# Kernel tuning notes

Hardware: AMD Instinct MI355X
Metric: run time of the kernel (lower is better)

The kernel has to match this reference:

```python
import jax, jax.numpy as jnp
import numpy as np

# CRPConfig defaults
KAPPA = 1.0
C = 0.95
ALPHA = 0.05
EPS = 1e-8
T_MAX = 32
MARGIN_FACTOR = 2.0

B, I, HD, L = 512, 1024, 2048, 1000


def setup_inputs() -> dict:
    key = jax.random.key(0)
    k0, k1, k2, k3 = jax.random.split(key, 4)
    x = jax.random.normal(k0, (B, I), jnp.float32)
    # kaiming-like scaling keeps activations numerically sane
    RIH = jax.random.normal(k1, (I, HD), jnp.float32) * np.float32(1.0 / np.sqrt(I))
    RH = jax.random.normal(k2, (HD, HD), jnp.float32) * np.float32(1.0 / np.sqrt(HD))
    RHL = jax.random.normal(k3, (HD, L), jnp.float32) * np.float32(1.0 / np.sqrt(HD))
    BH = jnp.zeros((HD,), jnp.float32)
    BL = jnp.zeros((L,), jnp.float32)
    MIH = jnp.ones((I, HD), jnp.float32)
    MH = jnp.ones((HD, HD), jnp.float32)
    MHL = jnp.ones((HD, L), jnp.float32)
    return {"x": x, "RIH": RIH, "RH": RH, "RHL": RHL, "BH": BH, "BL": BL,
            "MIH": MIH, "MH": MH, "MHL": MHL}


def _crp_forward(x, RIH, RH, RHL, BH, BL, MIH, MH, MHL):
    # build weights
    W_IH = RIH * MIH                      # [I, H]
    W_HL = RHL * MHL                      # [H, L]
    RHm = RH * MH                         # [H, H]
    # normalize so max column L1 <= c (value only; straight-through grad)
    col_l1 = jnp.abs(RHm).sum(axis=0)
    scale = C / jnp.maximum(col_l1.max(), EPS)
    W_H = jax.lax.stop_gradient(RHm * scale) + RHm - jax.lax.stop_gradient(RHm)

    rho = 1.0 - KAPPA + KAPPA * C
    denom = max(1e-12, 1.0 - rho)
    whl_inf = jnp.abs(W_HL).sum(axis=0).max()
    gamma_coef = whl_inf * (rho / denom)

    drive = x @ W_IH + BH                 # constant across steps, [B, H]
    Bsz = x.shape[0]
    Hs0 = jnp.zeros((Bsz, HD), x.dtype)
    active0 = jnp.ones((Bsz,), jnp.bool_)
    tau0 = jnp.full((Bsz,), T_MAX, jnp.int32)
    cert0 = jnp.zeros((Bsz,), jnp.bool_)
    logits_tau0 = jnp.zeros((Bsz, L), x.dtype)

    def step(carry, t):
        Hs, active, tau, certified, logits_tau = carry
        pre = Hs @ W_H + drive
        act = jnp.where(pre >= 0, pre, ALPHA * pre)      # LeakyReLU
        H_cand = (1.0 - KAPPA) * Hs + KAPPA * act
        H_next = jnp.where(active[:, None], H_cand, Hs)
        logits = H_next @ W_HL + BL
        # certification
        dH = jnp.max(jnp.abs(H_next - Hs), axis=1)       # H_prev == Hs
        Gamma = gamma_coef * dH
        top2 = jax.lax.top_k(logits, 2)[0]
        margin = top2[:, 0] - top2[:, 1]
        newly = active & (margin > MARGIN_FACTOR * Gamma)
        tau = jnp.where(newly, t, tau)
        certified = certified | newly
        logits_tau = jnp.where(newly[:, None], logits, logits_tau)
        active = active & (~newly)
        return (H_next, active, tau, certified, logits_tau), None

    ts = jnp.arange(1, T_MAX + 1, dtype=jnp.int32)
    (Hf, active, tau, certified, logits_tau), _ = jax.lax.scan(
        step, (Hs0, active0, tau0, cert0, logits_tau0), ts)

    never = ~certified
    logits_last = Hf @ W_HL + BL
    logits_tau = jnp.where(never[:, None], logits_last, logits_tau)
    return logits_tau


def reference(x, RIH, RH, RHL, BH, BL, MIH, MH, MHL):
    return _crp_forward(x, RIH, RH, RHL, BH, BL, MIH, MH, MHL)
```

## Files before the change

### kernel.cpp

```cpp
#include <hip/hip_runtime.h>

typedef __attribute__((ext_vector_type(8))) short short8;
typedef __attribute__((ext_vector_type(4))) float f32x4;

static constexpr int BN    = 512;
static constexpr int ID    = 1024;
static constexpr int HDm   = 2048;
static constexpr int LD    = 1000;
static constexpr int TMAXc = 32;
static constexpr float ALPHAc = 0.05f;

__device__ __forceinline__ unsigned short f2bf(float x) {
    unsigned u = __float_as_uint(x);
    u += 0x7fffu + ((u >> 16) & 1u);
    return (unsigned short)(u >> 16);
}
__device__ __forceinline__ float bf2f(unsigned short h) {
    return __uint_as_float(((unsigned)h) << 16);
}
__device__ __forceinline__ void split2(float x, unsigned short& hi, unsigned short& lo) {
    hi = f2bf(x);
    lo = f2bf(x - bf2f(hi));
}

template<bool SPLITA>
__device__ __forceinline__ void tile64x32(
    const float* __restrict__ Af,
    const unsigned short* __restrict__ Ahi, const unsigned short* __restrict__ Alo,
    int lda, int row0,
    const unsigned short* __restrict__ BThi, const unsigned short* __restrict__ BTlo,
    int ldk, int col0, int K, char* lds, f32x4& acc, int& s_out, int& p_out)
{
    char* Ah = lds;
    char* Al = lds + 16384;
    char* Bh = lds + 32768;
    char* Bl = lds + 40960;
    const int t = threadIdx.x, lane = t & 63, w = t >> 6;
    const int s = w & 7, p = w >> 3;
    s_out = s; p_out = p;
    f32x4 z = {0.f, 0.f, 0.f, 0.f};
    acc = z;

    const int ar = t >> 4, ac = (t & 15) << 3;
    const int br = t >> 5, bc = (t & 31) << 2;
    const int asb = (ar * 256 + ac * 2) ^ ((ar & 15) << 4);
    const int bsb = (br * 256 + bc * 2) ^ ((br & 15) << 4);
    const float* Ap = SPLITA ? (Af + (size_t)(row0 + ar) * lda + ac) : nullptr;
    const unsigned short* Ahp = SPLITA ? nullptr : (Ahi + (size_t)(row0 + ar) * lda + ac);
    const unsigned short* Alp = SPLITA ? nullptr : (Alo + (size_t)(row0 + ar) * lda + ac);
    const unsigned short* Bhp = BThi + (size_t)(col0 + br) * ldk + bc;
    const unsigned short* Blp = BTlo + (size_t)(col0 + br) * ldk + bc;

    const int frow = s >> 1, fcol = s & 1;
    const int arow = frow * 16 + (lane & 15);
    const int colr = fcol * 16 + (lane & 15);
    const int ab0 = arow * 256, bb0 = colr * 256;
    const int axor = (arow & 15) << 4, bxor = (colr & 15) << 4;
    const int kwin = p * 128 + ((lane >> 4) << 4);

    float4 af0a, af0b, af1a, af1b;
    uint4 ah0, al0, ah1, al1;
    if constexpr (SPLITA) {
        af0a = *(const float4*)(Ap);       af0b = *(const float4*)(Ap + 4);
        af1a = *(const float4*)(Ap + 128); af1b = *(const float4*)(Ap + 132);
    } else {
        ah0 = *(const uint4*)(Ahp);       al0 = *(const uint4*)(Alp);
        ah1 = *(const uint4*)(Ahp + 128); al1 = *(const uint4*)(Alp + 128);
    }
    uint2 bh0 = *(const uint2*)(Bhp),       bl0 = *(const uint2*)(Blp);
    uint2 bh1 = *(const uint2*)(Bhp + 128), bl1 = *(const uint2*)(Blp + 128);

    for (int k0 = 0; k0 < K; k0 += 128) {
        uint4 awh, awl;
        if constexpr (SPLITA) {
            unsigned short h[8], l[8];
            const float vv[8] = {af0a.x, af0a.y, af0a.z, af0a.w,
                                 af0b.x, af0b.y, af0b.z, af0b.w};
#pragma unroll
            for (int i = 0; i < 8; ++i) split2(vv[i], h[i], l[i]);
            awh = make_uint4((unsigned)h[0] | ((unsigned)h[1] << 16),
                             (unsigned)h[2] | ((unsigned)h[3] << 16),
                             (unsigned)h[4] | ((unsigned)h[5] << 16),
                             (unsigned)h[6] | ((unsigned)h[7] << 16));
            awl = make_uint4((unsigned)l[0] | ((unsigned)l[1] << 16),
                             (unsigned)l[2] | ((unsigned)l[3] << 16),
                             (unsigned)l[4] | ((unsigned)l[5] << 16),
                             (unsigned)l[6] | ((unsigned)l[7] << 16));
        } else { awh = ah0; awl = al0; }
        const uint2 bwh = bh0, bwl = bl0;
        __syncthreads();
        *(uint4*)(Ah + asb) = awh;
        *(uint4*)(Al + asb) = awl;
        *(uint2*)(Bh + bsb) = bwh;
        *(uint2*)(Bl + bsb) = bwl;
        if constexpr (SPLITA) { af0a = af1a; af0b = af1b; } else { ah0 = ah1; al0 = al1; }
        bh0 = bh1; bl0 = bl1;
        if (k0 + 256 < K) {
            if constexpr (SPLITA) {
                af1a = *(const float4*)(Ap + k0 + 256);
                af1b = *(const float4*)(Ap + k0 + 260);
            } else {
                ah1 = *(const uint4*)(Ahp + k0 + 256);
                al1 = *(const uint4*)(Alp + k0 + 256);
            }
            bh1 = *(const uint2*)(Bhp + k0 + 256);
            bl1 = *(const uint2*)(Blp + k0 + 256);
        }
        __syncthreads();
#pragma unroll
        for (int ks = 0; ks < 2; ++ks) {
            const int kb = kwin + ks * 64;
            short8 bh = *(const short8*)(Bh + ((bb0 + kb) ^ bxor));
            short8 bl = *(const short8*)(Bl + ((bb0 + kb) ^ bxor));
            short8 ah = *(const short8*)(Ah + ((ab0 + kb) ^ axor));
            short8 al = *(const short8*)(Al + ((ab0 + kb) ^ axor));
            acc = __builtin_amdgcn_mfma_f32_16x16x32_bf16(ah, bh, acc, 0, 0, 0);
            acc = __builtin_amdgcn_mfma_f32_16x16x32_bf16(al, bh, acc, 0, 0, 0);
            acc = __builtin_amdgcn_mfma_f32_16x16x32_bf16(ah, bl, acc, 0, 0, 0);
        }
    }
}

__device__ __forceinline__ void tile32x32(
    const unsigned short* __restrict__ Ahi, const unsigned short* __restrict__ Alo, int row0,
    const unsigned short* __restrict__ BThi, const unsigned short* __restrict__ BTlo,
    int col0, char* lds, f32x4& acc, int& s_out, int& p_out)
{
    char* Ah = lds;
    char* Al = lds + 8192;
    char* Bh = lds + 16384;
    char* Bl = lds + 24576;
    const int t = threadIdx.x, lane = t & 63, w = t >> 6;
    const int s = w & 3, p = w >> 2;
    s_out = s; p_out = p;
    f32x4 z = {0.f, 0.f, 0.f, 0.f};
    acc = z;

    const int ar = t >> 5, ac = (t & 31) << 2;
    const int asb = (ar * 256 + ac * 2) ^ ((ar & 15) << 4);
    const unsigned short* Ahp = Ahi + (size_t)(row0 + ar) * HDm + ac;
    const unsigned short* Alp = Alo + (size_t)(row0 + ar) * HDm + ac;
    const unsigned short* Bhp = BThi + (size_t)(col0 + ar) * HDm + ac;
    const unsigned short* Blp = BTlo + (size_t)(col0 + ar) * HDm + ac;

    const int frow = s >> 1, fcol = s & 1;
    const int arow = frow * 16 + (lane & 15);
    const int colr = fcol * 16 + (lane & 15);
    const int ab0 = arow * 256, bb0 = colr * 256;
    const int axor = (arow & 15) << 4, bxor = (colr & 15) << 4;
    const int kwin = p * 64 + ((lane >> 4) << 4);

    uint2 ah0 = *(const uint2*)(Ahp),       al0 = *(const uint2*)(Alp);
    uint2 bh0 = *(const uint2*)(Bhp),       bl0 = *(const uint2*)(Blp);
    uint2 ah1 = *(const uint2*)(Ahp + 128), al1 = *(const uint2*)(Alp + 128);
    uint2 bh1 = *(const uint2*)(Bhp + 128), bl1 = *(const uint2*)(Blp + 128);

    for (int k0 = 0; k0 < HDm; k0 += 128) {
        const uint2 awh = ah0, awl = al0, bwh = bh0, bwl = bl0;
        __syncthreads();
        *(uint2*)(Ah + asb) = awh;
        *(uint2*)(Al + asb) = awl;
        *(uint2*)(Bh + asb) = bwh;
        *(uint2*)(Bl + asb) = bwl;
        ah0 = ah1; al0 = al1; bh0 = bh1; bl0 = bl1;
        if (k0 + 256 < HDm) {
            ah1 = *(const uint2*)(Ahp + k0 + 256);
            al1 = *(const uint2*)(Alp + k0 + 256);
            bh1 = *(const uint2*)(Bhp + k0 + 256);
            bl1 = *(const uint2*)(Blp + k0 + 256);
        }
        __syncthreads();
        const int kb = kwin;
        short8 bh = *(const short8*)(Bh + ((bb0 + kb) ^ bxor));
        short8 bl = *(const short8*)(Bl + ((bb0 + kb) ^ bxor));
        short8 ah = *(const short8*)(Ah + ((ab0 + kb) ^ axor));
        short8 al = *(const short8*)(Al + ((ab0 + kb) ^ axor));
        acc = __builtin_amdgcn_mfma_f32_16x16x32_bf16(ah, bh, acc, 0, 0, 0);
        acc = __builtin_amdgcn_mfma_f32_16x16x32_bf16(al, bh, acc, 0, 0, 0);
        acc = __builtin_amdgcn_mfma_f32_16x16x32_bf16(ah, bl, acc, 0, 0, 0);
    }
}

__global__ void k_init(int* active, int* cnt, float* scal,
                       float* margS, float* drift, int* fresh)
{
    int i = blockIdx.x * blockDim.x + threadIdx.x;
    if (i < 2 * BN) {
        active[i] = 1;
        margS[i] = 3.4e38f;
        drift[i] = 0.f;
        fresh[i] = 1;
    }
    if (i < 16) cnt[i] = 64;
    if (i < 8) scal[i] = 0.f;
}

__global__ __launch_bounds__(256) void k_colsum_wh(const float* __restrict__ RH,
                                                   const float* __restrict__ MH,
                                                   float* __restrict__ part)
{
    const int colTile = blockIdx.x >> 3, rs = blockIdx.x & 7;
    const int col = colTile * 64 + (threadIdx.x & 63);
    const int rq = threadIdx.x >> 6;
    const int r0 = rs * 256;
    float s = 0.f;
    for (int i = r0 + rq; i < r0 + 256; i += 4)
        s += fabsf(RH[(size_t)i * HDm + col] * MH[(size_t)i * HDm + col]);
    __shared__ float red[4][64];
    red[rq][threadIdx.x & 63] = s;
    __syncthreads();
    if (threadIdx.x < 64)
        part[(size_t)rs * HDm + col] = red[0][threadIdx.x] + red[1][threadIdx.x] +
                                       red[2][threadIdx.x] + red[3][threadIdx.x];
}

__global__ __launch_bounds__(256) void k_colsum_whl(const float* __restrict__ RHL,
                                                    const float* __restrict__ MHL,
                                                    float* __restrict__ part)
{
    const int colTile = blockIdx.x >> 3, rs = blockIdx.x & 7;
    const int col = colTile * 64 + (threadIdx.x & 63);
    const int rq = threadIdx.x >> 6;
    const int r0 = rs * 256;
    float s = 0.f;
    if (col < LD) {
        for (int i = r0 + rq; i < r0 + 256; i += 4)
            s += fabsf(RHL[(size_t)i * LD + col] * MHL[(size_t)i * LD + col]);
    }
    __shared__ float red[4][64];
    red[rq][threadIdx.x & 63] = s;
    __syncthreads();
    if (threadIdx.x < 64)
        part[(size_t)rs * 1024 + col] = red[0][threadIdx.x] + red[1][threadIdx.x] +
                                        red[2][threadIdx.x] + red[3][threadIdx.x];
}

__global__ __launch_bounds__(1024) void k_scalars(const float* __restrict__ part_wh,
                                                  const float* __restrict__ part_whl,
                                                  float* scal)
{
    float m1 = 0.f, m2 = 0.f;
    for (int c = threadIdx.x; c < HDm; c += 1024) {
        float s = 0.f;
#pragma unroll
        for (int k = 0; k < 8; ++k) s += part_wh[(size_t)k * HDm + c];
        m1 = fmaxf(m1, s);
    }
    {
        const int c = threadIdx.x;
        if (c < 1024) {
            float s = 0.f;
#pragma unroll
            for (int k = 0; k < 8; ++k) s += part_whl[(size_t)k * 1024 + c];
            m2 = fmaxf(m2, s);
        }
    }
#pragma unroll
    for (int off = 1; off < 64; off <<= 1) {
        m1 = fmaxf(m1, __shfl_xor(m1, off));
        m2 = fmaxf(m2, __shfl_xor(m2, off));
    }
    __shared__ float r1[16], r2[16];
    if ((threadIdx.x & 63) == 0) { r1[threadIdx.x >> 6] = m1; r2[threadIdx.x >> 6] = m2; }
    __syncthreads();
    if (threadIdx.x == 0) {
        float a = 0.f, b = 0.f;
#pragma unroll
        for (int i = 0; i < 16; ++i) { a = fmaxf(a, r1[i]); b = fmaxf(b, r2[i]); }
        scal[2] = 0.95f / fmaxf(a, 1e-8f);
        scal[3] = b * 19.f;
    }
}

__global__ __launch_bounds__(256) void k_wsplit(
    const float* __restrict__ R, const float* __restrict__ M,
    unsigned short* __restrict__ Ohi, unsigned short* __restrict__ Olo,
    int NR, int NC, int NCp, const float* __restrict__ scal, int scidx)
{
    __shared__ float T[64][65];
    const int nct = NCp >> 6;
    const int c0 = (blockIdx.x % nct) << 6;
    const int r0 = (blockIdx.x / nct) << 6;
    const float s = (scidx >= 0) ? scal[scidx] : 1.f;
    const int t = threadIdx.x;
    const int ir = t >> 2, ics = (t & 3) << 4;
#pragma unroll
    for (int i = 0; i < 16; ++i) {
        const int c = c0 + ics + i;
        float v = 0.f;
        if (c < NC) {
            const size_t idx = (size_t)(r0 + ir) * NC + c;
            v = R[idx] * M[idx] * s;
        }
        T[ir][ics + i] = v;
    }
    __syncthreads();
    const int oc = t >> 2, ors = (t & 3) << 4;
    unsigned short hb[16], lb[16];
#pragma unroll
    for (int i = 0; i < 16; ++i) split2(T[ors + i][oc], hb[i], lb[i]);
    const size_t base = (size_t)(c0 + oc) * NR + r0 + ors;
    uint4 v;
    v.x = hb[0] | ((unsigned)hb[1] << 16);  v.y = hb[2] | ((unsigned)hb[3] << 16);
    v.z = hb[4] | ((unsigned)hb[5] << 16);  v.w = hb[6] | ((unsigned)hb[7] << 16);
    *(uint4*)(Ohi + base) = v;
    v.x = hb[8] | ((unsigned)hb[9] << 16);  v.y = hb[10] | ((unsigned)hb[11] << 16);
    v.z = hb[12] | ((unsigned)hb[13] << 16); v.w = hb[14] | ((unsigned)hb[15] << 16);
    *(uint4*)(Ohi + base + 8) = v;
    v.x = lb[0] | ((unsigned)lb[1] << 16);  v.y = lb[2] | ((unsigned)lb[3] << 16);
    v.z = lb[4] | ((unsigned)lb[5] << 16);  v.w = lb[6] | ((unsigned)lb[7] << 16);
    *(uint4*)(Olo + base) = v;
    v.x = lb[8] | ((unsigned)lb[9] << 16);  v.y = lb[10] | ((unsigned)lb[11] << 16);
    v.z = lb[12] | ((unsigned)lb[13] << 16); v.w = lb[14] | ((unsigned)lb[15] << 16);
    *(uint4*)(Olo + base + 8) = v;
}

__global__ __launch_bounds__(1024, 8) void k_drive_mfma(
    const float* __restrict__ x,
    const unsigned short* __restrict__ WIHThi, const unsigned short* __restrict__ WIHTlo,
    const float* __restrict__ BH, float* __restrict__ drive)
{
    __shared__ char lds[49152];
    f32x4 acc;
    int s, p;
    const int row0 = (blockIdx.x >> 6) * 64, col0 = (blockIdx.x & 63) * 32;
    tile64x32<true>(x, nullptr, nullptr, ID, row0, WIHThi, WIHTlo, ID, col0, ID,
                    lds, acc, s, p);
    const int lane = threadIdx.x & 63;
    __syncthreads();
    f32x4* red = (f32x4*)lds;
    if (p == 1) red[s * 64 + lane] = acc;
    __syncthreads();
    if (p == 0) {
        f32x4 o = red[s * 64 + lane];
        acc += o;
        const int frow = s >> 1, fcol = s & 1;
        const int gc = col0 + fcol * 16 + (lane & 15);
        const int gr0 = row0 + frow * 16 + ((lane >> 4) << 2);
        const float bh = BH[gc];
#pragma unroll
        for (int r = 0; r < 4; ++r)
            drive[(size_t)(gr0 + r) * HDm + gc] = acc[r] + bh;
    }
}

__global__ __launch_bounds__(1024, 8) void k_p1(
    const unsigned short* __restrict__ WHThi, const unsigned short* __restrict__ WHTlo,
    const float* __restrict__ drive,
    unsigned short* __restrict__ HAhi, unsigned short* __restrict__ HAlo,
    unsigned short* __restrict__ HBhi, unsigned short* __restrict__ HBlo,
    const float* __restrict__ logits, float* __restrict__ out,
    int* __restrict__ active, int* __restrict__ cnt, const float* __restrict__ scal,
    float* __restrict__ dhp, const float* __restrict__ m1p, const float* __restrict__ m2p,
    float* __restrict__ margS, float* __restrict__ drift, const int* __restrict__ fresh,
    int t)
{
    __shared__ char lds[49152];
    __shared__ int sact[64], snew[64];
    __shared__ int s_cnt;
    const int pp = (t - 1) & 1, pc = t & 1;
    {
        const int* cp = cnt + pp * 8;
        int sum = 0;
#pragma unroll
        for (int i = 0; i < 8; ++i) sum += cp[i];
        if (sum == 0) return;
    }
    const int bid = blockIdx.x, tid = threadIdx.x;
    const int rt = bid >> 6, row0m = rt << 6, col0 = (bid & 63) * 32;
    const int* actP = active + pp * BN;
    int* actC = active + pc * BN;
    const unsigned short* Hshi = (t & 1) ? HAhi : HBhi;
    const unsigned short* Hslo = (t & 1) ? HAlo : HBlo;
    unsigned short* Hnhi = (t & 1) ? HBhi : HAhi;
    unsigned short* Hnlo = (t & 1) ? HBlo : HAlo;
    const float* dhpP = dhp + (size_t)pp * BN * 64;
    float* dhpC = dhp + (size_t)pc * BN * 64;
    const float* margSP = margS + pp * BN;
    float* margSC = margS + pc * BN;
    const float* driftP = drift + pp * BN;
    float* driftC = drift + pc * BN;
    const int* freshP = fresh + pp * BN;

    if (t > 1) {
        const float gamma2 = 2.f * scal[3];
        const int rl = tid >> 4, j = tid & 15;
        const int r = row0m + rl;
        const int act = actP[r];
        const int fr = freshP[r];
        float dh = fmaxf(fmaxf(dhpP[(size_t)r * 64 + j],      dhpP[(size_t)r * 64 + 16 + j]),
                         fmaxf(dhpP[(size_t)r * 64 + 32 + j], dhpP[(size_t)r * 64 + 48 + j]));
        float M1 = m1p[(size_t)r * 32 + j], M2 = m2p[(size_t)r * 32 + j];
        {
            float o1 = m1p[(size_t)r * 32 + 16 + j], o2 = m2p[(size_t)r * 32 + 16 + j];
            if (o1 > M1) { M2 = fmaxf(M1, o2); M1 = o1; }
            else M2 = fmaxf(M2, o1);
        }
#pragma unroll
        for (int off = 1; off < 16; off <<= 1) {
            dh = fmaxf(dh, __shfl_xor(dh, off));
            float o1 = __shfl_xor(M1, off), o2 = __shfl_xor(M2, off);
            if (o1 > M1) { M2 = fmaxf(M1, o2); M1 = o1; }
            else M2 = fmaxf(M2, o1);
        }
        if (j == 0) {
            const float marg = M1 - M2;
            int nw = fr && act && (marg > gamma2 * dh);
            snew[rl] = nw;
            sact[rl] = act && !nw;
            margSC[r] = fr ? marg : margSP[r];
            driftC[r] = fr ? 0.f : (driftP[r] + dh);
        }
    } else if (tid < 64) {
        sact[tid] = 1; snew[tid] = 0;
    }
    __syncthreads();
    if (tid < 64) {
        unsigned long long b = __ballot(sact[tid] != 0);
        actC[row0m + tid] = sact[tid];
        if (tid == 0) {
            s_cnt = __popcll(b);
            (cnt + pc * 8)[rt] = s_cnt;
        }
    }
    if (t > 1 && (bid & 63) == 0) {
        for (int rl2 = 0; rl2 < 64; ++rl2) {
            if (snew[rl2]) {
                const float* lr = logits + (size_t)(row0m + rl2) * LD;
                float* orow = out + (size_t)(row0m + rl2) * LD;
                for (int jj = tid; jj < LD; jj += 1024) orow[jj] = lr[jj];
            }
        }
    }
    __syncthreads();
    if (s_cnt == 0) return;

    f32x4 acc;
    int s, p;
    tile64x32<false>(nullptr, Hshi, Hslo, HDm, row0m, WHThi, WHTlo, HDm, col0, HDm,
                     lds, acc, s, p);
    const int lane = tid & 63;
    __syncthreads();
    f32x4* red = (f32x4*)lds;
    if (p == 1) red[s * 64 + lane] = acc;
    __syncthreads();
    float (*sdh)[2] = (float(*)[2])(lds + 16384);
    if (p == 0) {
        f32x4 o = red[s * 64 + lane];
        acc += o;
        const int frow = s >> 1, fcol = s & 1;
        const int gc = col0 + fcol * 16 + (lane & 15);
        const int gr0 = row0m + frow * 16 + ((lane >> 4) << 2);
        float dh4[4];
#pragma unroll
        for (int r = 0; r < 4; ++r) {
            const int gr = gr0 + r;
            const size_t idx = (size_t)gr * HDm + gc;
            const unsigned short oh = Hshi[idx], ol = Hslo[idx];
            const float old = bf2f(oh) + bf2f(ol);
            const int a = sact[gr - row0m];
            unsigned short nh, nl;
            if (a) {
                const float pre = acc[r] + drive[idx];
                const float av = pre >= 0.f ? pre : ALPHAc * pre;
                split2(av, nh, nl);
            } else { nh = oh; nl = ol; }
            Hnhi[idx] = nh; Hnlo[idx] = nl;
            dh4[r] = fabsf((bf2f(nh) + bf2f(nl)) - old);
        }
#pragma unroll
        for (int off = 1; off < 16; off <<= 1)
#pragma unroll
            for (int r = 0; r < 4; ++r)
                dh4[r] = fmaxf(dh4[r], __shfl_xor(dh4[r], off));
        if ((lane & 15) == 0) {
            const int rl0 = frow * 16 + ((lane >> 4) << 2);
#pragma unroll
            for (int r = 0; r < 4; ++r) sdh[rl0 + r][fcol] = dh4[r];
        }
    }
    __syncthreads();
    if (tid < 64) {
        float d = fmaxf(sdh[tid][0], sdh[tid][1]);
        dhpC[(size_t)(row0m + tid) * 64 + (bid & 63)] = d;
    }
}

__global__ __launch_bounds__(1024, 8) void k_p2(
    const unsigned short* __restrict__ WHLThi, const unsigned short* __restrict__ WHLTlo,
    const float* __restrict__ BL,
    const unsigned short* __restrict__ HAhi, const unsigned short* __restrict__ HAlo,
    const unsigned short* __restrict__ HBhi, const unsigned short* __restrict__ HBlo,
    float* __restrict__ logits, const int* __restrict__ active, const int* __restrict__ cnt,
    float* __restrict__ m1p, float* __restrict__ m2p, const float* __restrict__ scal,
    const float* __restrict__ dhp, const float* __restrict__ margS,
    const float* __restrict__ drift, int* __restrict__ fresh, int t)
{
    __shared__ char lds[46080];
    __shared__ int sposs[32];
    __shared__ int s_go;
    const int pc = t & 1;
    {
        const int* cp = cnt + pc * 8;
        int sum = 0;
#pragma unroll
        for (int i = 0; i < 8; ++i) sum += cp[i];
        if (sum == 0) return;
    }
    const int bid = blockIdx.x, tid = threadIdx.x;
    const unsigned short* Hnhi = (t & 1) ? HBhi : HAhi;
    const unsigned short* Hnlo = (t & 1) ? HBlo : HAlo;
    const int* actC = active + pc * BN;
    const float* dhpC = dhp + (size_t)pc * BN * 64;
    const float* margSc = margS + pc * BN;
    const float* driftc = drift + pc * BN;
    int* freshC = fresh + pc * BN;
    const int row0 = (bid >> 5) * 32, col0 = (bid & 31) * 32;

    {
        const int rr = tid >> 5, j = tid & 31;
        const int r = row0 + rr;
        float d = fmaxf(dhpC[(size_t)r * 64 + j], dhpC[(size_t)r * 64 + 32 + j]);
#pragma unroll
        for (int off = 1; off < 32; off <<= 1) d = fmaxf(d, __shfl_xor(d, off));
        if (j == 0) {
            const int act = actC[r];
            int poss;
            if (t == TMAXc) poss = act;
            else {
                const float whl = scal[3] * (1.f / 19.f);
                poss = act && (margSc[r] + 2.f * whl * (driftc[r] + d) >
                               0.99f * 38.f * whl * d);
            }
            sposs[rr] = poss;
        }
    }
    __syncthreads();
    if (tid < 64) {
        int v = (tid < 32) ? sposs[tid] : 0;
        unsigned long long b = __ballot(v != 0);
        if (tid == 0) s_go = (b != 0ull);
    }
    __syncthreads();
    if (tid < 32) freshC[row0 + tid] = s_go;
    if (!s_go) return;

    f32x4 acc;
    int s, p;
    tile32x32(Hnhi, Hnlo, row0, WHLThi, WHLTlo, col0, lds, acc, s, p);
    const int lane = tid & 63;
    __syncthreads();
    f32x4* red = (f32x4*)lds;
    if (p > 0) red[(p - 1) * 256 + s * 64 + lane] = acc;
    __syncthreads();
    float (*st1)[2] = (float(*)[2])(lds + 12288);
    float (*st2)[2] = (float(*)[2])(lds + 12544);
    if (p == 0) {
#pragma unroll
        for (int q = 0; q < 3; ++q) {
            f32x4 o = red[q * 256 + s * 64 + lane];
            acc += o;
        }
        const int frow = s >> 1, fcol = s & 1;
        const int gc = col0 + fcol * 16 + (lane & 15);
        const int gr0 = row0 + frow * 16 + ((lane >> 4) << 2);
        const bool okc = gc < LD;
        const float blv = okc ? BL[gc] : 0.f;
        float m1a[4], m2a[4];
#pragma unroll
        for (int r = 0; r < 4; ++r) {
            const float v = acc[r] + blv;
            if (okc) logits[(size_t)(gr0 + r) * LD + gc] = v;
            m1a[r] = okc ? v : -3.4e38f;
            m2a[r] = -3.4e38f;
        }
#pragma unroll
        for (int off = 1; off < 16; off <<= 1) {
#pragma unroll
            for (int r = 0; r < 4; ++r) {
                float o1 = __shfl_xor(m1a[r], off);
                float o2 = __shfl_xor(m2a[r], off);
                if (o1 > m1a[r]) { m2a[r] = fmaxf(m1a[r], o2); m1a[r] = o1; }
                else m2a[r] = fmaxf(m2a[r], o1);
            }
        }
        if ((lane & 15) == 0) {
            const int rl0 = frow * 16 + ((lane >> 4) << 2);
#pragma unroll
            for (int r = 0; r < 4; ++r) {
                st1[rl0 + r][fcol] = m1a[r];
                st2[rl0 + r][fcol] = m2a[r];
            }
        }
    }
    __syncthreads();
    if (tid < 32) {
        float M1 = st1[tid][0], M2 = st2[tid][0];
        {
            float o1 = st1[tid][1], o2 = st2[tid][1];
            if (o1 > M1) { M2 = fmaxf(M1, o2); M1 = o1; }
            else M2 = fmaxf(M2, o1);
        }
        m1p[(size_t)(row0 + tid) * 32 + (bid & 31)] = M1;
        m2p[(size_t)(row0 + tid) * 32 + (bid & 31)] = M2;
    }
}

__global__ __launch_bounds__(1024) void k_tail(
    const float* __restrict__ logits, const int* __restrict__ active,
    float* __restrict__ out)
{
    const int row0 = blockIdx.x * 64;
    for (int rl = 0; rl < 64; ++rl) {
        const int r = row0 + rl;
        if (active[r] && active[BN + r]) {
            const float* lr = logits + (size_t)r * LD;
            float* orow = out + (size_t)r * LD;
            for (int jj = threadIdx.x; jj < LD; jj += 1024) orow[jj] = lr[jj];
        }
    }
}

extern "C" void kernel_launch(void* const* d_in, const int* in_sizes, int n_in,
                              void* d_out, int out_size, void* d_ws, size_t ws_size,
                              hipStream_t stream)
{
    const float* x   = (const float*)d_in[0];
    const float* RIH = (const float*)d_in[1];
    const float* RH  = (const float*)d_in[2];
    const float* RHL = (const float*)d_in[3];
    const float* BH  = (const float*)d_in[4];
    const float* BL  = (const float*)d_in[5];
    const float* MIH = (const float*)d_in[6];
    const float* MH  = (const float*)d_in[7];
    const float* MHL = (const float*)d_in[8];
    float* out = (float*)d_out;
    char* w = (char*)d_ws;

    unsigned short* WHThi = (unsigned short*)(w);
    unsigned short* WHTlo = (unsigned short*)(w + 8388608);
    unsigned short* WXhi  = (unsigned short*)(w + 16777216);
    unsigned short* WXlo  = (unsigned short*)(w + 20971520);
    float* drive  = (float*)(w + 25165824);
    unsigned short* HAhi = (unsigned short*)(w + 29360128);
    unsigned short* HAlo = (unsigned short*)(w + 31457280);
    unsigned short* HBhi = (unsigned short*)(w + 33554432);
    unsigned short* HBlo = (unsigned short*)(w + 35651584);
    float* logits = (float*)(w + 37748736);
    float* scal   = (float*)(w + 39796736);
    int*   active = (int*)(w + 39796800);
    int*   cnt    = (int*)(w + 39800896);
    float* dhp    = (float*)(w + 39800960);
    float* m1p    = (float*)(w + 40063104);
    float* m2p    = (float*)(w + 40128640);
    float* margS  = (float*)(w + 40194176);
    float* drift  = (float*)(w + 40198272);
    int*   fresh  = (int*)(w + 40202368);

    k_init<<<4, 256, 0, stream>>>(active, cnt, scal, margS, drift, fresh);
    k_colsum_wh<<<256, 256, 0, stream>>>(RH, MH, dhp);
    k_colsum_whl<<<128, 256, 0, stream>>>(RHL, MHL, m1p);
    k_scalars<<<1, 1024, 0, stream>>>(dhp, m1p, scal);
    k_wsplit<<<512, 256, 0, stream>>>(RIH, MIH, WXhi, WXlo, ID, HDm, HDm, scal, -1);
    k_drive_mfma<<<512, 1024, 0, stream>>>(x, WXhi, WXlo, BH, drive);
    k_wsplit<<<1024, 256, 0, stream>>>(RH, MH, WHThi, WHTlo, HDm, HDm, HDm, scal, 2);
    k_wsplit<<<512, 256, 0, stream>>>(RHL, MHL, WXhi, WXlo, HDm, LD, 1024, scal, -1);
    (void)hipMemsetAsync(HAhi, 0, 4194304, stream);

    for (int t = 1; t <= TMAXc; ++t) {
        k_p1<<<512, 1024, 0, stream>>>(WHThi, WHTlo, drive, HAhi, HAlo, HBhi, HBlo,
                                       logits, out, active, cnt, scal, dhp, m1p, m2p,
                                       margS, drift, fresh, t);
        k_p2<<<512, 1024, 0, stream>>>(WXhi, WXlo, BL, HAhi, HAlo, HBhi, HBlo,
                                       logits, active, cnt, m1p, m2p, scal,
                                       dhp, margS, drift, fresh, t);
    }
    k_tail<<<8, 1024, 0, stream>>>(logits, active, out);
}
```

Before: 1.357 ms.

## Store H and weights as pre-swizzled LDS tile images loaded via global_load_lds

The recurrent state H and the W_H / W_HL weight splits are now kept in global memory as contiguous, pre-swizzled tile images that match the LDS layout. The per-step GEMM tiles can then copy them straight into LDS with 16-byte global_load_lds, skipping the register staging and per-thread swizzled stores. A new k_wsplit_img kernel builds the weight images, and k_p1 writes H in image layout through himg_off. The trade-off is that the register-level prefetch double-buffering is dropped, so each k-chunk now loads and then waits on a barrier.

```diff
diff --git a/kernel.cpp b/kernel.cpp
--- a/kernel.cpp
+++ b/kernel.cpp
@@ -23,11 +23,21 @@
     lo = f2bf(x - bf2f(hi));
 }
 
-template<bool SPLITA>
-__device__ __forceinline__ void tile64x32(
-    const float* __restrict__ Af,
-    const unsigned short* __restrict__ Ahi, const unsigned short* __restrict__ Alo,
-    int lda, int row0,
+__device__ __forceinline__ void gload16(const void* g, void* l) {
+    __builtin_amdgcn_global_load_lds(
+        (const __attribute__((address_space(1))) unsigned int*)g,
+        (__attribute__((address_space(3))) unsigned int*)l, 16, 0, 0);
+}
+
+
+__device__ __forceinline__ size_t himg_off(int gr, int gc) {
+    const int rt = gr >> 6, ar = gr & 63, kc = gc >> 7, ac = gc & 127;
+    const int byte = (ar * 256 + ac * 2) ^ ((ar & 15) << 4);
+    return ((size_t)(rt * 16 + kc) << 14) + byte;
+}
+
+__device__ __forceinline__ void tile64_drive(
+    const float* __restrict__ Af, int lda, int row0,
     const unsigned short* __restrict__ BThi, const unsigned short* __restrict__ BTlo,
     int ldk, int col0, int K, char* lds, f32x4& acc, int& s_out, int& p_out)
 {
@@ -45,9 +55,7 @@
     const int br = t >> 5, bc = (t & 31) << 2;
     const int asb = (ar * 256 + ac * 2) ^ ((ar & 15) << 4);
     const int bsb = (br * 256 + bc * 2) ^ ((br & 15) << 4);
-    const float* Ap = SPLITA ? (Af + (size_t)(row0 + ar) * lda + ac) : nullptr;
-    const unsigned short* Ahp = SPLITA ? nullptr : (Ahi + (size_t)(row0 + ar) * lda + ac);
-    const unsigned short* Alp = SPLITA ? nullptr : (Alo + (size_t)(row0 + ar) * lda + ac);
+    const float* Ap = Af + (size_t)(row0 + ar) * lda + ac;
     const unsigned short* Bhp = BThi + (size_t)(col0 + br) * ldk + bc;
     const unsigned short* Blp = BTlo + (size_t)(col0 + br) * ldk + bc;
 
@@ -58,51 +66,36 @@
     const int axor = (arow & 15) << 4, bxor = (colr & 15) << 4;
     const int kwin = p * 128 + ((lane >> 4) << 4);
 
-    float4 af0a, af0b, af1a, af1b;
-    uint4 ah0, al0, ah1, al1;
-    if constexpr (SPLITA) {
-        af0a = *(const float4*)(Ap);       af0b = *(const float4*)(Ap + 4);
-        af1a = *(const float4*)(Ap + 128); af1b = *(const float4*)(Ap + 132);
-    } else {
-        ah0 = *(const uint4*)(Ahp);       al0 = *(const uint4*)(Alp);
-        ah1 = *(const uint4*)(Ahp + 128); al1 = *(const uint4*)(Alp + 128);
-    }
+    float4 af0a = *(const float4*)(Ap),       af0b = *(const float4*)(Ap + 4);
+    float4 af1a = *(const float4*)(Ap + 128), af1b = *(const float4*)(Ap + 132);
     uint2 bh0 = *(const uint2*)(Bhp),       bl0 = *(const uint2*)(Blp);
     uint2 bh1 = *(const uint2*)(Bhp + 128), bl1 = *(const uint2*)(Blp + 128);
 
     for (int k0 = 0; k0 < K; k0 += 128) {
-        uint4 awh, awl;
-        if constexpr (SPLITA) {
-            unsigned short h[8], l[8];
-            const float vv[8] = {af0a.x, af0a.y, af0a.z, af0a.w,
-                                 af0b.x, af0b.y, af0b.z, af0b.w};
-#pragma unroll
-            for (int i = 0; i < 8; ++i) split2(vv[i], h[i], l[i]);
-            awh = make_uint4((unsigned)h[0] | ((unsigned)h[1] << 16),
-                             (unsigned)h[2] | ((unsigned)h[3] << 16),
-                             (unsigned)h[4] | ((unsigned)h[5] << 16),
-                             (unsigned)h[6] | ((unsigned)h[7] << 16));
-            awl = make_uint4((unsigned)l[0] | ((unsigned)l[1] << 16),
-                             (unsigned)l[2] | ((unsigned)l[3] << 16),
-                             (unsigned)l[4] | ((unsigned)l[5] << 16),
-                             (unsigned)l[6] | ((unsigned)l[7] << 16));
-        } else { awh = ah0; awl = al0; }
+        unsigned short h[8], l[8];
+        const float vv[8] = {af0a.x, af0a.y, af0a.z, af0a.w,
+                             af0b.x, af0b.y, af0b.z, af0b.w};
+#pragma unroll
+        for (int i = 0; i < 8; ++i) split2(vv[i], h[i], l[i]);
+        uint4 awh = make_uint4((unsigned)h[0] | ((unsigned)h[1] << 16),
+                               (unsigned)h[2] | ((unsigned)h[3] << 16),
+                               (unsigned)h[4] | ((unsigned)h[5] << 16),
+                               (unsigned)h[6] | ((unsigned)h[7] << 16));
+        uint4 awl = make_uint4((unsigned)l[0] | ((unsigned)l[1] << 16),
+                               (unsigned)l[2] | ((unsigned)l[3] << 16),
+                               (unsigned)l[4] | ((unsigned)l[5] << 16),
+                               (unsigned)l[6] | ((unsigned)l[7] << 16));
         const uint2 bwh = bh0, bwl = bl0;
         __syncthreads();
         *(uint4*)(Ah + asb) = awh;
         *(uint4*)(Al + asb) = awl;
         *(uint2*)(Bh + bsb) = bwh;
         *(uint2*)(Bl + bsb) = bwl;
-        if constexpr (SPLITA) { af0a = af1a; af0b = af1b; } else { ah0 = ah1; al0 = al1; }
+        af0a = af1a; af0b = af1b;
         bh0 = bh1; bl0 = bl1;
         if (k0 + 256 < K) {
-            if constexpr (SPLITA) {
-                af1a = *(const float4*)(Ap + k0 + 256);
-                af1b = *(const float4*)(Ap + k0 + 260);
-            } else {
-                ah1 = *(const uint4*)(Ahp + k0 + 256);
-                al1 = *(const uint4*)(Alp + k0 + 256);
-            }
+            af1a = *(const float4*)(Ap + k0 + 256);
+            af1b = *(const float4*)(Ap + k0 + 260);
             bh1 = *(const uint2*)(Bhp + k0 + 256);
             bl1 = *(const uint2*)(Blp + k0 + 256);
         }
@@ -121,10 +114,54 @@
     }
 }
 
-__device__ __forceinline__ void tile32x32(
-    const unsigned short* __restrict__ Ahi, const unsigned short* __restrict__ Alo, int row0,
-    const unsigned short* __restrict__ BThi, const unsigned short* __restrict__ BTlo,
-    int col0, char* lds, f32x4& acc, int& s_out, int& p_out)
+__device__ __forceinline__ void tile64_img(
+    const char* __restrict__ Ahi, const char* __restrict__ Alo,
+    const char* __restrict__ Bhi, const char* __restrict__ Blo,
+    char* lds, f32x4& acc, int& s_out, int& p_out)
+{
+    char* Ah = lds;
+    char* Al = lds + 16384;
+    char* Bh = lds + 32768;
+    char* Bl = lds + 40960;
+    const int t = threadIdx.x, lane = t & 63, w = t >> 6;
+    const int s = w & 7, p = w >> 3;
+    s_out = s; p_out = p;
+    f32x4 z = {0.f, 0.f, 0.f, 0.f};
+    acc = z;
+
+    const int frow = s >> 1, fcol = s & 1;
+    const int arow = frow * 16 + (lane & 15);
+    const int colr = fcol * 16 + (lane & 15);
+    const int ab0 = arow * 256, bb0 = colr * 256;
+    const int axor = (arow & 15) << 4, bxor = (colr & 15) << 4;
+    const int kwin = p * 128 + ((lane >> 4) << 4);
+    const int t16 = t * 16;
+
+    for (int kc = 0; kc < 16; ++kc) {
+        __syncthreads();
+        gload16(Ahi + ((size_t)kc << 14) + t16, Ah + (w << 10));
+        gload16(Alo + ((size_t)kc << 14) + t16, Al + (w << 10));
+        if (w < 8) gload16(Bhi + ((size_t)kc << 13) + t16, Bh + (w << 10));
+        else       gload16(Blo + ((size_t)kc << 13) + t16 - 8192, Bl + ((w - 8) << 10));
+        __syncthreads();
+#pragma unroll
+        for (int ks = 0; ks < 2; ++ks) {
+            const int kb = kwin + ks * 64;
+            short8 bh = *(const short8*)(Bh + ((bb0 + kb) ^ bxor));
+            short8 bl = *(const short8*)(Bl + ((bb0 + kb) ^ bxor));
+            short8 ah = *(const short8*)(Ah + ((ab0 + kb) ^ axor));
+            short8 al = *(const short8*)(Al + ((ab0 + kb) ^ axor));
+            acc = __builtin_amdgcn_mfma_f32_16x16x32_bf16(ah, bh, acc, 0, 0, 0);
+            acc = __builtin_amdgcn_mfma_f32_16x16x32_bf16(al, bh, acc, 0, 0, 0);
+            acc = __builtin_amdgcn_mfma_f32_16x16x32_bf16(ah, bl, acc, 0, 0, 0);
+        }
+    }
+}
+
+__device__ __forceinline__ void tile32_img(
+    const char* __restrict__ Ahi, const char* __restrict__ Alo,
+    const char* __restrict__ Bhi, const char* __restrict__ Blo,
+    char* lds, f32x4& acc, int& s_out, int& p_out)
 {
     char* Ah = lds;
     char* Al = lds + 8192;
@@ -136,38 +173,22 @@
     f32x4 z = {0.f, 0.f, 0.f, 0.f};
     acc = z;
 
-    const int ar = t >> 5, ac = (t & 31) << 2;
-    const int asb = (ar * 256 + ac * 2) ^ ((ar & 15) << 4);
-    const unsigned short* Ahp = Ahi + (size_t)(row0 + ar) * HDm + ac;
-    const unsigned short* Alp = Alo + (size_t)(row0 + ar) * HDm + ac;
-    const unsigned short* Bhp = BThi + (size_t)(col0 + ar) * HDm + ac;
-    const unsigned short* Blp = BTlo + (size_t)(col0 + ar) * HDm + ac;
-
     const int frow = s >> 1, fcol = s & 1;
     const int arow = frow * 16 + (lane & 15);
     const int colr = fcol * 16 + (lane & 15);
     const int ab0 = arow * 256, bb0 = colr * 256;
     const int axor = (arow & 15) << 4, bxor = (colr & 15) << 4;
     const int kwin = p * 64 + ((lane >> 4) << 4);
-
-    uint2 ah0 = *(const uint2*)(Ahp),       al0 = *(const uint2*)(Alp);
-    uint2 bh0 = *(const uint2*)(Bhp),       bl0 = *(const uint2*)(Blp);
-    uint2 ah1 = *(const uint2*)(Ahp + 128), al1 = *(const uint2*)(Alp + 128);
-    uint2 bh1 = *(const uint2*)(Bhp + 128), bl1 = *(const uint2*)(Blp + 128);
-
-    for (int k0 = 0; k0 < HDm; k0 += 128) {
-        const uint2 awh = ah0, awl = al0, bwh = bh0, bwl = bl0;
+    const int t16 = t * 16;
+
+    for (int kc = 0; kc < 16; ++kc) {
         __syncthreads();
-        *(uint2*)(Ah + asb) = awh;
-        *(uint2*)(Al + asb) = awl;
-        *(uint2*)(Bh + asb) = bwh;
-        *(uint2*)(Bl + asb) = bwl;
-        ah0 = ah1; al0 = al1; bh0 = bh1; bl0 = bl1;
-        if (k0 + 256 < HDm) {
-            ah1 = *(const uint2*)(Ahp + k0 + 256);
-            al1 = *(const uint2*)(Alp + k0 + 256);
-            bh1 = *(const uint2*)(Bhp + k0 + 256);
-            bl1 = *(const uint2*)(Blp + k0 + 256);
+        if (w < 8) {
+            gload16(Ahi + ((size_t)kc << 14) + t16, Ah + (w << 10));
+            gload16(Bhi + ((size_t)kc << 13) + t16, Bh + (w << 10));
+        } else {
+            gload16(Alo + ((size_t)kc << 14) + t16 - 8192, Al + ((w - 8) << 10));
+            gload16(Blo + ((size_t)kc << 13) + t16 - 8192, Bl + ((w - 8) << 10));
         }
         __syncthreads();
         const int kb = kwin;
@@ -315,6 +336,31 @@
     *(uint4*)(Olo + base + 8) = v;
 }
 
+__global__ __launch_bounds__(256) void k_wsplit_img(
+    const float* __restrict__ R, const float* __restrict__ M,
+    char* __restrict__ imghi, char* __restrict__ imglo,
+    int NC, int nkc, const float* __restrict__ scal, int scidx)
+{
+    const int ct = blockIdx.x / nkc, kc = blockIdx.x % nkc;
+    const float s = (scidx >= 0) ? scal[scidx] : 1.f;
+    char* hi = imghi + ((size_t)(ct * nkc + kc) << 13);
+    char* lo = imglo + ((size_t)(ct * nkc + kc) << 13);
+#pragma unroll
+    for (int i = 0; i < 16; ++i) {
+        const int idx = i * 256 + threadIdx.x;
+        const int br = idx & 31, bc = idx >> 5;
+        const int c = ct * 32 + br;
+        const int k = kc * 128 + bc;
+        float v = 0.f;
+        if (c < NC) { const size_t a = (size_t)k * NC + c; v = R[a] * M[a] * s; }
+        unsigned short h, l;
+        split2(v, h, l);
+        const int byte = (br * 256 + bc * 2) ^ ((br & 15) << 4);
+        *(unsigned short*)(hi + byte) = h;
+        *(unsigned short*)(lo + byte) = l;
+    }
+}
+
 __global__ __launch_bounds__(1024, 8) void k_drive_mfma(
     const float* __restrict__ x,
     const unsigned short* __restrict__ WIHThi, const unsigned short* __restrict__ WIHTlo,
@@ -324,8 +370,7 @@
     f32x4 acc;
     int s, p;
     const int row0 = (blockIdx.x >> 6) * 64, col0 = (blockIdx.x & 63) * 32;
-    tile64x32<true>(x, nullptr, nullptr, ID, row0, WIHThi, WIHTlo, ID, col0, ID,
-                    lds, acc, s, p);
+    tile64_drive(x, ID, row0, WIHThi, WIHTlo, ID, col0, ID, lds, acc, s, p);
     const int lane = threadIdx.x & 63;
     __syncthreads();
     f32x4* red = (f32x4*)lds;
@@ -345,10 +390,10 @@
 }
 
 __global__ __launch_bounds__(1024, 8) void k_p1(
-    const unsigned short* __restrict__ WHThi, const unsigned short* __restrict__ WHTlo,
+    const char* __restrict__ WHhi, const char* __restrict__ WHlo,
     const float* __restrict__ drive,
-    unsigned short* __restrict__ HAhi, unsigned short* __restrict__ HAlo,
-    unsigned short* __restrict__ HBhi, unsigned short* __restrict__ HBlo,
+    char* __restrict__ HAhi, char* __restrict__ HAlo,
+    char* __restrict__ HBhi, char* __restrict__ HBlo,
     const float* __restrict__ logits, float* __restrict__ out,
     int* __restrict__ active, int* __restrict__ cnt, const float* __restrict__ scal,
     float* __restrict__ dhp, const float* __restrict__ m1p, const float* __restrict__ m2p,
@@ -370,10 +415,10 @@
     const int rt = bid >> 6, row0m = rt << 6, col0 = (bid & 63) * 32;
     const int* actP = active + pp * BN;
     int* actC = active + pc * BN;
-    const unsigned short* Hshi = (t & 1) ? HAhi : HBhi;
-    const unsigned short* Hslo = (t & 1) ? HAlo : HBlo;
-    unsigned short* Hnhi = (t & 1) ? HBhi : HAhi;
-    unsigned short* Hnlo = (t & 1) ? HBlo : HAlo;
+    const char* Hshi = (t & 1) ? HAhi : HBhi;
+    const char* Hslo = (t & 1) ? HAlo : HBlo;
+    char* Hnhi = (t & 1) ? HBhi : HAhi;
+    char* Hnlo = (t & 1) ? HBlo : HAlo;
     const float* dhpP = dhp + (size_t)pp * BN * 64;
     float* dhpC = dhp + (size_t)pc * BN * 64;
     const float* margSP = margS + pp * BN;
@@ -437,8 +482,9 @@
 
     f32x4 acc;
     int s, p;
-    tile64x32<false>(nullptr, Hshi, Hslo, HDm, row0m, WHThi, WHTlo, HDm, col0, HDm,
-                     lds, acc, s, p);
+    tile64_img(Hshi + ((size_t)(rt * 16) << 14), Hslo + ((size_t)(rt * 16) << 14),
+               WHhi + ((size_t)((bid & 63) * 16) << 13), WHlo + ((size_t)((bid & 63) * 16) << 13),
+               lds, acc, s, p);
     const int lane = tid & 63;
     __syncthreads();
     f32x4* red = (f32x4*)lds;
@@ -455,17 +501,19 @@
 #pragma unroll
         for (int r = 0; r < 4; ++r) {
             const int gr = gr0 + r;
-            const size_t idx = (size_t)gr * HDm + gc;
-            const unsigned short oh = Hshi[idx], ol = Hslo[idx];
+            const size_t ia = himg_off(gr, gc);
+            const unsigned short oh = *(const unsigned short*)(Hshi + ia);
+            const unsigned short ol = *(const unsigned short*)(Hslo + ia);
             const float old = bf2f(oh) + bf2f(ol);
             const int a = sact[gr - row0m];
             unsigned short nh, nl;
             if (a) {
-                const float pre = acc[r] + drive[idx];
+                const float pre = acc[r] + drive[(size_t)gr * HDm + gc];
                 const float av = pre >= 0.f ? pre : ALPHAc * pre;
                 split2(av, nh, nl);
             } else { nh = oh; nl = ol; }
-            Hnhi[idx] = nh; Hnlo[idx] = nl;
+            *(unsigned short*)(Hnhi + ia) = nh;
+            *(unsigned short*)(Hnlo + ia) = nl;
             dh4[r] = fabsf((bf2f(nh) + bf2f(nl)) - old);
         }
 #pragma unroll
@@ -487,16 +535,16 @@
 }
 
 __global__ __launch_bounds__(1024, 8) void k_p2(
-    const unsigned short* __restrict__ WHLThi, const unsigned short* __restrict__ WHLTlo,
+    const char* __restrict__ WLhi, const char* __restrict__ WLlo,
     const float* __restrict__ BL,
-    const unsigned short* __restrict__ HAhi, const unsigned short* __restrict__ HAlo,
-    const unsigned short* __restrict__ HBhi, const unsigned short* __restrict__ HBlo,
+    const char* __restrict__ HAhi, const char* __restrict__ HAlo,
+    const char* __restrict__ HBhi, const char* __restrict__ HBlo,
     float* __restrict__ logits, const int* __restrict__ active, const int* __restrict__ cnt,
     float* __restrict__ m1p, float* __restrict__ m2p, const float* __restrict__ scal,
     const float* __restrict__ dhp, const float* __restrict__ margS,
     const float* __restrict__ drift, int* __restrict__ fresh, int t)
 {
-    __shared__ char lds[46080];
+    __shared__ char lds[33280];
     __shared__ int sposs[32];
     __shared__ int s_go;
     const int pc = t & 1;
@@ -508,8 +556,8 @@
         if (sum == 0) return;
     }
     const int bid = blockIdx.x, tid = threadIdx.x;
-    const unsigned short* Hnhi = (t & 1) ? HBhi : HAhi;
-    const unsigned short* Hnlo = (t & 1) ? HBlo : HAlo;
+    const char* Hnhi = (t & 1) ? HBhi : HAhi;
+    const char* Hnlo = (t & 1) ? HBlo : HAlo;
     const int* actC = active + pc * BN;
     const float* dhpC = dhp + (size_t)pc * BN * 64;
     const float* margSc = margS + pc * BN;
@@ -545,9 +593,14 @@
     if (tid < 32) freshC[row0 + tid] = s_go;
     if (!s_go) return;
 
+    const int rt2 = bid >> 5;
+    const char* Ahi = Hnhi + ((size_t)((rt2 >> 1) * 16) << 14) + ((rt2 & 1) << 13);
+    const char* Alo = Hnlo + ((size_t)((rt2 >> 1) * 16) << 14) + ((rt2 & 1) << 13);
     f32x4 acc;
     int s, p;
-    tile32x32(Hnhi, Hnlo, row0, WHLThi, WHLTlo, col0, lds, acc, s, p);
+    tile32_img(Ahi, Alo,
+               WLhi + ((size_t)((bid & 31) * 16) << 13), WLlo + ((size_t)((bid & 31) * 16) << 13),
+               lds, acc, s, p);
     const int lane = tid & 63;
     __syncthreads();
     f32x4* red = (f32x4*)lds;
@@ -637,15 +690,15 @@
     float* out = (float*)d_out;
     char* w = (char*)d_ws;
 
-    unsigned short* WHThi = (unsigned short*)(w);
-    unsigned short* WHTlo = (unsigned short*)(w + 8388608);
-    unsigned short* WXhi  = (unsigned short*)(w + 16777216);
-    unsigned short* WXlo  = (unsigned short*)(w + 20971520);
-    float* drive  = (float*)(w + 25165824);
-    unsigned short* HAhi = (unsigned short*)(w + 29360128);
-    unsigned short* HAlo = (unsigned short*)(w + 31457280);
-    unsigned short* HBhi = (unsigned short*)(w + 33554432);
-    unsigned short* HBlo = (unsigned short*)(w + 35651584);
+    char* WHhi = w;
+    char* WHlo = w + 8388608;
+    char* WXhi = w + 16777216;
+    char* WXlo = w + 20971520;
+    float* drive = (float*)(w + 25165824);
+    char* HAhi = w + 29360128;
+    char* HAlo = w + 31457280;
+    char* HBhi = w + 33554432;
+    char* HBlo = w + 35651584;
     float* logits = (float*)(w + 37748736);
     float* scal   = (float*)(w + 39796736);
     int*   active = (int*)(w + 39796800);
@@ -661,14 +714,16 @@
     k_colsum_wh<<<256, 256, 0, stream>>>(RH, MH, dhp);
     k_colsum_whl<<<128, 256, 0, stream>>>(RHL, MHL, m1p);
     k_scalars<<<1, 1024, 0, stream>>>(dhp, m1p, scal);
-    k_wsplit<<<512, 256, 0, stream>>>(RIH, MIH, WXhi, WXlo, ID, HDm, HDm, scal, -1);
-    k_drive_mfma<<<512, 1024, 0, stream>>>(x, WXhi, WXlo, BH, drive);
-    k_wsplit<<<1024, 256, 0, stream>>>(RH, MH, WHThi, WHTlo, HDm, HDm, HDm, scal, 2);
-    k_wsplit<<<512, 256, 0, stream>>>(RHL, MHL, WXhi, WXlo, HDm, LD, 1024, scal, -1);
+    k_wsplit<<<512, 256, 0, stream>>>(RIH, MIH, (unsigned short*)WXhi,
+                                      (unsigned short*)WXlo, ID, HDm, HDm, scal, -1);
+    k_drive_mfma<<<512, 1024, 0, stream>>>(x, (const unsigned short*)WXhi,
+                                           (const unsigned short*)WXlo, BH, drive);
+    k_wsplit_img<<<1024, 256, 0, stream>>>(RH, MH, WHhi, WHlo, HDm, 16, scal, 2);
+    k_wsplit_img<<<512, 256, 0, stream>>>(RHL, MHL, WXhi, WXlo, LD, 16, scal, -1);
     (void)hipMemsetAsync(HAhi, 0, 4194304, stream);
 
     for (int t = 1; t <= TMAXc; ++t) {
-        k_p1<<<512, 1024, 0, stream>>>(WHThi, WHTlo, drive, HAhi, HAlo, HBhi, HBlo,
+        k_p1<<<512, 1024, 0, stream>>>(WHhi, WHlo, drive, HAhi, HAlo, HBhi, HBlo,
                                        logits, out, active, cnt, scal, dhp, m1p, m2p,
                                        margS, drift, fresh, t);
         k_p2<<<512, 1024, 0, stream>>>(WXhi, WXlo, BL, HAhi, HAlo, HBhi, HBlo,
```

New measurement: 1.336 ms (median of 2 runs). Within noise of the previous version (-1.6%).
